# Kernel optimization log

Hardware: AMD Instinct MI355X
Metric: run time of the kernel (lower is better)

## Reference

```python
import jax, jax.numpy as jnp
import numpy as np

D_MODEL, D_INNER, D_STATE, D_CONV, DT_RANK = 2048, 4096, 16, 4, 128
B, T = 2, 1024


def setup_inputs() -> dict:
    key = jax.random.key(0)
    ks = jax.random.split(key, 8)
    dt_init_std = DT_RANK ** -0.5
    # dt bias init per the torch code: inv softplus of dt in [dt_min, dt_max]
    dt = jnp.exp(jax.random.uniform(ks[6], (D_INNER,)) * (np.log(0.1) - np.log(0.001)) + np.log(0.001))
    dt = jnp.clip(dt, 1e-4, None)
    dt_proj_b = dt + jnp.log(-jnp.expm1(-dt))
    A_log = jnp.log(jnp.tile(jnp.arange(1, D_STATE + 1, dtype=jnp.float32)[None, :], (D_INNER, 1)))
    return {
        "x": jax.random.normal(ks[0], (B, T, D_MODEL), jnp.float32),
        "h": jnp.zeros((B, D_INNER, D_STATE), jnp.float32),
        "conv_cache": jnp.zeros((B, D_INNER, D_CONV - 1), jnp.float32),
        "in_proj_w": jax.random.normal(ks[1], (2 * D_INNER, D_MODEL), jnp.float32) * 0.02,
        "conv_w": jax.random.normal(ks[2], (D_INNER, D_CONV), jnp.float32) * (1.0 / np.sqrt(D_CONV)),
        "conv_b": jnp.zeros((D_INNER,), jnp.float32),
        "x_proj_w": jax.random.normal(ks[3], (DT_RANK + 2 * D_STATE, D_INNER), jnp.float32) * 0.02,
        "dt_proj_w": jax.random.uniform(ks[4], (D_INNER, DT_RANK), jnp.float32, -dt_init_std, dt_init_std),
        "dt_proj_b": dt_proj_b,
        "A_log": A_log,
        "D_param": jnp.ones((D_INNER,), jnp.float32),
        "out_proj_w": jax.random.normal(ks[5], (D_MODEL, D_INNER), jnp.float32) * 0.02,
    }


def _forward(x, h, conv_cache, in_proj_w, conv_w, conv_b, x_proj_w,
             dt_proj_w, dt_proj_b, A_log, D_param, out_proj_w):
    Tlen = x.shape[1]
    xz = x @ in_proj_w.T                                  # (B,T,2*d_inner)
    xi, z = jnp.split(xz, 2, axis=-1)
    # causal depthwise conv with cache: concat history then valid conv
    xc = jnp.concatenate([jnp.swapaxes(conv_cache, 1, 2), xi], axis=1)  # (B,T+3,d_inner)
    new_conv_cache = jnp.swapaxes(xc[:, -(D_CONV - 1):, :], 1, 2)       # (B,d_inner,3)
    xconv = sum(xc[:, k:k + Tlen, :] * conv_w[:, k] for k in range(D_CONV)) + conv_b
    xs = jax.nn.silu(xconv)                               # (B,T,d_inner)
    # SSM params per step
    dbc = xs @ x_proj_w.T                                 # (B,T,dt_rank+2n)
    delta, Bm, Cm = jnp.split(dbc, [DT_RANK, DT_RANK + D_STATE], axis=-1)
    delta = jax.nn.softplus(delta @ dt_proj_w.T + dt_proj_b)  # (B,T,d_inner)
    A = -jnp.exp(A_log)                                   # (d_inner,n)
    dA = jnp.exp(jnp.einsum('btd,dn->btdn', delta, A))    # (B,T,d,n)
    dBx = jnp.einsum('btd,btn,btd->btdn', delta, Bm, xs)  # (B,T,d,n)

    def step(hc, inp):
        dA_t, dBx_t, C_t = inp
        hc = dA_t * hc + dBx_t                            # (B,d,n)
        return hc, jnp.einsum('bdn,bn->bd', hc, C_t)

    h_last, ys = jax.lax.scan(
        step, h,
        (jnp.moveaxis(dA, 1, 0), jnp.moveaxis(dBx, 1, 0), jnp.moveaxis(Cm, 1, 0)))
    y = jnp.moveaxis(ys, 0, 1) + D_param * xs             # (B,T,d_inner)
    out = (y * jax.nn.silu(z)) @ out_proj_w.T             # (B,T,d_model)
    return out, h_last, new_conv_cache


def reference(x, h, conv_cache, in_proj_w, conv_w, conv_b, x_proj_w,
              dt_proj_w, dt_proj_b, A_log, D_param, out_proj_w):
    return _forward(x, h, conv_cache, in_proj_w, conv_w, conv_b, x_proj_w,
                    dt_proj_w, dt_proj_b, A_log, D_param, out_proj_w)
```

## Files before the change

kernel.cpp:

```cpp
#include <hip/hip_runtime.h>
#include <hip/hip_bf16.h>
#include <math.h>

#define D_MODEL 2048
#define D_INNER 4096
#define D_STATE 16
#define D_CONV  4
#define DT_RANK 128
#define NB      2
#define TT      1024
#define M_TOT   (NB * TT)
#define NC      16
#define CL      64
#define TC      16

typedef __bf16 bf16x8_t __attribute__((ext_vector_type(8)));
typedef float  f32x4_t  __attribute__((ext_vector_type(4)));

__global__ __launch_bounds__(256) void fused_cast(
    const float* __restrict__ x,  const float* __restrict__ wi,
    const float* __restrict__ wo, const float* __restrict__ wx,
    const float* __restrict__ wdt,
    __bf16* __restrict__ x16,  __bf16* __restrict__ wi16,
    __bf16* __restrict__ wo16, __bf16* __restrict__ wx16,
    __bf16* __restrict__ wdt16, __bf16* __restrict__ dbc16,
    __bf16* __restrict__ out16)
{
    const size_t g = (size_t)blockIdx.x * 256 + threadIdx.x;
    const float* src; __bf16* dst; size_t off;
    if      (g < 524288)  { src = x;   dst = x16;   off = g; }
    else if (g < 2621440) { src = wi;  dst = wi16;  off = g - 524288; }
    else if (g < 3670016) { src = wo;  dst = wo16;  off = g - 2621440; }
    else if (g < 3801088) { off = g - 3670016; dst = wx16;
                            src = (g < 3751936) ? wx : nullptr; }
    else if (g < 3866624) { src = wdt; dst = wdt16; off = g - 3801088; }
    else if (g < 3948544) { src = nullptr; dst = dbc16; off = g - 3866624; }
    else                  { src = nullptr; dst = out16; off = g - 3948544; }

    bf16x8_t v;
    if (src) {
        const float4 f0 = ((const float4*)src)[2 * off];
        const float4 f1 = ((const float4*)src)[2 * off + 1];
        v[0] = (__bf16)f0.x; v[1] = (__bf16)f0.y; v[2] = (__bf16)f0.z; v[3] = (__bf16)f0.w;
        v[4] = (__bf16)f1.x; v[5] = (__bf16)f1.y; v[6] = (__bf16)f1.z; v[7] = (__bf16)f1.w;
    } else {
        v = (bf16x8_t)(__bf16)0.f;
    }
    ((bf16x8_t*)dst)[off] = v;
}

template <int EPI, int KSTEP, typename OutT>
__global__ __launch_bounds__(256) void gemm_bf16_nt(
    const __bf16* __restrict__ A, int lda,
    const __bf16* __restrict__ W, int ldw,
    OutT* __restrict__ C, int ldc,
    int Kloop, int Nmax, const float* __restrict__ bias)
{
    __shared__ __bf16 As[128 * KSTEP];
    __shared__ __bf16 Bs[128 * KSTEP];

    const int tid  = threadIdx.x;
    const int wave = tid >> 6;
    const int lane = tid & 63;
    const int m0 = blockIdx.y * 128;
    const int n0 = blockIdx.x * 128;
    const int mw = (wave >> 1) * 64;
    const int nw = (wave & 1) * 64;
    const int koff = blockIdx.z * Kloop;

    f32x4_t acc[4][4] = {};

    const int g0 = wave * 2;
    const int rA = g0 * 16 + (lane >> 2);
    const int kk = (lane & 3) * 8;

    const __bf16* gA0 = A + (size_t)(m0 + rA) * lda + kk + koff;
    const __bf16* gA1 = gA0 + (size_t)16 * lda;
    const __bf16* gB0 = W + (size_t)(n0 + rA) * ldw + kk + koff;
    const __bf16* gB1 = gB0 + (size_t)16 * ldw;

    __bf16* lA0 = &As[(size_t)g0 * 512];
    __bf16* lA1 = &As[(size_t)(g0 + 1) * 512];
    __bf16* lB0 = &Bs[(size_t)g0 * 512];
    __bf16* lB1 = &Bs[(size_t)(g0 + 1) * 512];

    const int fr = lane & 15;
    const int fk = (lane >> 4) * 8;

    for (int k0 = 0; k0 < Kloop; k0 += KSTEP) {
#pragma unroll
        for (int p = 0; p < KSTEP / 32; p++) {
            const int kp = k0 + p * 32;
            const int lp = p * 4096;
            __builtin_amdgcn_global_load_lds(
                (const __attribute__((address_space(1))) void*)(gA0 + kp),
                (__attribute__((address_space(3))) void*)(lA0 + lp), 16, 0, 0);
            __builtin_amdgcn_global_load_lds(
                (const __attribute__((address_space(1))) void*)(gA1 + kp),
                (__attribute__((address_space(3))) void*)(lA1 + lp), 16, 0, 0);
            __builtin_amdgcn_global_load_lds(
                (const __attribute__((address_space(1))) void*)(gB0 + kp),
                (__attribute__((address_space(3))) void*)(lB0 + lp), 16, 0, 0);
            __builtin_amdgcn_global_load_lds(
                (const __attribute__((address_space(1))) void*)(gB1 + kp),
                (__attribute__((address_space(3))) void*)(lB1 + lp), 16, 0, 0);
        }
        __syncthreads();

#pragma unroll
        for (int p = 0; p < KSTEP / 32; p++) {
            const int lp = p * 4096;
            bf16x8_t av[4], bv[4];
#pragma unroll
            for (int mt = 0; mt < 4; mt++)
                av[mt] = *(const bf16x8_t*)&As[lp + (mw + mt * 16 + fr) * 32 + fk];
#pragma unroll
            for (int nt = 0; nt < 4; nt++)
                bv[nt] = *(const bf16x8_t*)&Bs[lp + (nw + nt * 16 + fr) * 32 + fk];

#pragma unroll
            for (int mt = 0; mt < 4; mt++)
#pragma unroll
                for (int nt = 0; nt < 4; nt++)
                    acc[mt][nt] = __builtin_amdgcn_mfma_f32_16x16x32_bf16(
                        av[mt], bv[nt], acc[mt][nt], 0, 0, 0);
        }
        __syncthreads();
    }

    const int cn = n0 + nw + (lane & 15);
    const int rb = m0 + mw + (lane >> 4) * 4;
#pragma unroll
    for (int mt = 0; mt < 4; mt++)
#pragma unroll
        for (int nt = 0; nt < 4; nt++) {
            const int n = cn + nt * 16;
            if (n >= Nmax) continue;
#pragma unroll
            for (int r = 0; r < 4; r++) {
                float v = acc[mt][nt][r];
                OutT* p = &C[(size_t)(rb + mt * 16 + r) * ldc + n];
                if (EPI == 1) {
                    v += bias[n];
                    v = (v > 20.f) ? v : log1pf(__expf(v));
                    *p = (OutT)v;
                } else if (EPI == 2) {
                    atomicAdd((float*)p, v);
                } else {
                    *p = (OutT)v;
                }
            }
        }
}

__global__ __launch_bounds__(256) void gemm_dt(
    const float* __restrict__ A,
    const __bf16* __restrict__ W,
    __bf16* __restrict__ C,
    const float* __restrict__ bias)
{
    __shared__ __bf16 As[128 * 32];
    __shared__ __bf16 Bs[128 * 32];

    const int tid  = threadIdx.x;
    const int wave = tid >> 6;
    const int lane = tid & 63;
    const int m0 = blockIdx.y * 128;
    const int n0 = blockIdx.x * 128;
    const int mw = (wave >> 1) * 64;
    const int nw = (wave & 1) * 64;

    f32x4_t acc[4][4] = {};

    const int g0 = wave * 2;
    const int rA = g0 * 16 + (lane >> 2);
    const int kk = (lane & 3) * 8;

    const float*  gA0 = A + (size_t)(m0 + rA) * 160 + kk;
    const float*  gA1 = gA0 + (size_t)16 * 160;
    const __bf16* gB0 = W + (size_t)(n0 + rA) * 128 + kk;
    const __bf16* gB1 = gB0 + (size_t)16 * 128;

    __bf16* lA0 = &As[(size_t)g0 * 512];
    __bf16* lA1 = &As[(size_t)(g0 + 1) * 512];
    __bf16* lB0 = &Bs[(size_t)g0 * 512];
    __bf16* lB1 = &Bs[(size_t)(g0 + 1) * 512];

    const int fr = lane & 15;
    const int fk = (lane >> 4) * 8;

    for (int k0 = 0; k0 < 128; k0 += 32) {
        const float4 a0 = *(const float4*)(gA0 + k0);
        const float4 a1 = *(const float4*)(gA0 + k0 + 4);
        const float4 a2 = *(const float4*)(gA1 + k0);
        const float4 a3 = *(const float4*)(gA1 + k0 + 4);
        bf16x8_t va, vb;
        va[0] = (__bf16)a0.x; va[1] = (__bf16)a0.y; va[2] = (__bf16)a0.z; va[3] = (__bf16)a0.w;
        va[4] = (__bf16)a1.x; va[5] = (__bf16)a1.y; va[6] = (__bf16)a1.z; va[7] = (__bf16)a1.w;
        vb[0] = (__bf16)a2.x; vb[1] = (__bf16)a2.y; vb[2] = (__bf16)a2.z; vb[3] = (__bf16)a2.w;
        vb[4] = (__bf16)a3.x; vb[5] = (__bf16)a3.y; vb[6] = (__bf16)a3.z; vb[7] = (__bf16)a3.w;
        ((bf16x8_t*)lA0)[lane] = va;
        ((bf16x8_t*)lA1)[lane] = vb;
        __builtin_amdgcn_global_load_lds(
            (const __attribute__((address_space(1))) void*)(gB0 + k0),
            (__attribute__((address_space(3))) void*)lB0, 16, 0, 0);
        __builtin_amdgcn_global_load_lds(
            (const __attribute__((address_space(1))) void*)(gB1 + k0),
            (__attribute__((address_space(3))) void*)lB1, 16, 0, 0);
        __syncthreads();

        bf16x8_t av[4], bv[4];
#pragma unroll
        for (int mt = 0; mt < 4; mt++)
            av[mt] = *(const bf16x8_t*)&As[(mw + mt * 16 + fr) * 32 + fk];
#pragma unroll
        for (int nt = 0; nt < 4; nt++)
            bv[nt] = *(const bf16x8_t*)&Bs[(nw + nt * 16 + fr) * 32 + fk];

#pragma unroll
        for (int mt = 0; mt < 4; mt++)
#pragma unroll
            for (int nt = 0; nt < 4; nt++)
                acc[mt][nt] = __builtin_amdgcn_mfma_f32_16x16x32_bf16(
                    av[mt], bv[nt], acc[mt][nt], 0, 0, 0);
        __syncthreads();
    }

    const int cn = n0 + nw + (lane & 15);
    const int rb = m0 + mw + (lane >> 4) * 4;
#pragma unroll
    for (int mt = 0; mt < 4; mt++)
#pragma unroll
        for (int nt = 0; nt < 4; nt++) {
            const int n = cn + nt * 16;
            const float bs = bias[n];
#pragma unroll
            for (int r = 0; r < 4; r++) {
                float v = acc[mt][nt][r] + bs;
                v = (v > 20.f) ? v : log1pf(__expf(v));
                C[(size_t)(rb + mt * 16 + r) * 4096 + n] = (__bf16)v;
            }
        }
}

__global__ __launch_bounds__(256) void conv_silu(
    const __bf16* __restrict__ xz16,
    const float* __restrict__ conv_cache,
    const float* __restrict__ conv_w,
    const float* __restrict__ conv_b,
    __bf16* __restrict__ xs16,
    float* __restrict__ cc_out)
{
    const int b  = blockIdx.z;
    const int d  = blockIdx.y * 256 + threadIdx.x;
    const int t0 = blockIdx.x * TC;

    const float4 w  = *(const float4*)&conv_w[d * 4];
    const float bias = conv_b[d];

    float v[TC + 3];
    if (t0 == 0) {
        v[0] = conv_cache[(b * D_INNER + d) * 3 + 0];
        v[1] = conv_cache[(b * D_INNER + d) * 3 + 1];
        v[2] = conv_cache[(b * D_INNER + d) * 3 + 2];
    } else {
        v[0] = (float)xz16[(size_t)(b * TT + t0 - 3) * 8192 + d];
        v[1] = (float)xz16[(size_t)(b * TT + t0 - 2) * 8192 + d];
        v[2] = (float)xz16[(size_t)(b * TT + t0 - 1) * 8192 + d];
    }
#pragma unroll
    for (int k = 0; k < TC; k++)
        v[k + 3] = (float)xz16[(size_t)(b * TT + t0 + k) * 8192 + d];

#pragma unroll
    for (int k = 0; k < TC; k++) {
        float c = v[k] * w.x + v[k + 1] * w.y + v[k + 2] * w.z + v[k + 3] * w.w + bias;
        float s = c / (1.f + __expf(-c));
        xs16[(size_t)(b * TT + t0 + k) * 4096 + d] = (__bf16)s;
    }

    if (t0 + TC == TT) {
        cc_out[(b * D_INNER + d) * 3 + 0] = v[TC];
        cc_out[(b * D_INNER + d) * 3 + 1] = v[TC + 1];
        cc_out[(b * D_INNER + d) * 3 + 2] = v[TC + 2];
    }
}

__global__ __launch_bounds__(256) void scan_phase_a(
    const __bf16* __restrict__ delta16,
    const float* __restrict__ dbc,
    const __bf16* __restrict__ xs16,
    const float* __restrict__ A_log,
    float* __restrict__ P,
    float* __restrict__ S)
{
    const int idx = blockIdx.x * 256 + threadIdx.x;
    const int sub = idx & 3;
    const int d   = (idx >> 2) & 4095;
    const int c   = (idx >> 14) & (NC - 1);
    const int b   = idx >> 18;

    const float4 Af = *(const float4*)&A_log[d * 16 + sub * 4];
    const float Ad0 = -__expf(Af.x), Ad1 = -__expf(Af.y);
    const float Ad2 = -__expf(Af.z), Ad3 = -__expf(Af.w);

    const int t0 = c * CL;
    const __bf16* pdelta = delta16 + (size_t)(b * TT + t0) * 4096 + d;
    const __bf16* px     = xs16 + (size_t)(b * TT + t0) * 4096 + d;
    const float*  pB     = dbc + ((size_t)b * TT + t0) * 160 + 128 + sub * 4;

    float h0 = 0.f, h1 = 0.f, h2 = 0.f, h3 = 0.f, sd = 0.f;
#pragma unroll 4
    for (int t = 0; t < CL; t++) {
        const float delta = (float)pdelta[(size_t)t * 4096];
        const float xv    = (float)px[(size_t)t * 4096];
        const float4 Bv   = *(const float4*)&pB[(size_t)t * 160];
        const float dx = delta * xv;
        h0 = __expf(delta * Ad0) * h0 + dx * Bv.x;
        h1 = __expf(delta * Ad1) * h1 + dx * Bv.y;
        h2 = __expf(delta * Ad2) * h2 + dx * Bv.z;
        h3 = __expf(delta * Ad3) * h3 + dx * Bv.w;
        sd += delta;
    }
    const size_t o = ((size_t)(b * NC + c) * 4096 + d) * 16 + sub * 4;
    *(float4*)&P[o] = make_float4(__expf(Ad0 * sd), __expf(Ad1 * sd),
                                  __expf(Ad2 * sd), __expf(Ad3 * sd));
    *(float4*)&S[o] = make_float4(h0, h1, h2, h3);
}

__global__ __launch_bounds__(256) void scan_phase_c(
    const __bf16* __restrict__ delta16,
    const __bf16* __restrict__ xz16,
    const float* __restrict__ dbc,
    const __bf16* __restrict__ xs16,
    const float* __restrict__ P,
    const float* __restrict__ S,
    const float* __restrict__ h_in,
    const float* __restrict__ A_log,
    const float* __restrict__ D_param,
    __bf16* __restrict__ ys16,
    float* __restrict__ h_out)
{
    const int idx = blockIdx.x * 256 + threadIdx.x;
    const int sub = idx & 3;
    const int d   = (idx >> 2) & 4095;
    const int c   = (idx >> 14) & (NC - 1);
    const int b   = idx >> 18;

    const float4 Af = *(const float4*)&A_log[d * 16 + sub * 4];
    const float Ad0 = -__expf(Af.x), Ad1 = -__expf(Af.y);
    const float Ad2 = -__expf(Af.z), Ad3 = -__expf(Af.w);
    const float Dp = D_param[d];

    float4 hf = *(const float4*)&h_in[((size_t)b * 4096 + d) * 16 + sub * 4];
    float h0 = hf.x, h1 = hf.y, h2 = hf.z, h3 = hf.w;
    for (int cc = 0; cc < c; cc++) {
        const size_t o2 = ((size_t)(b * NC + cc) * 4096 + d) * 16 + sub * 4;
        const float4 p = *(const float4*)&P[o2];
        const float4 s = *(const float4*)&S[o2];
        h0 = p.x * h0 + s.x;
        h1 = p.y * h1 + s.y;
        h2 = p.z * h2 + s.z;
        h3 = p.w * h3 + s.w;
    }

    const int t0 = c * CL;
    const __bf16* pdelta = delta16 + (size_t)(b * TT + t0) * 4096 + d;
    const __bf16* pz     = xz16 + (size_t)(b * TT + t0) * 8192 + 4096 + d;
    const __bf16* px     = xs16 + (size_t)(b * TT + t0) * 4096 + d;
    const float*  pB     = dbc + ((size_t)b * TT + t0) * 160 + 128 + sub * 4;
    const float*  pC     = pB + 16;
    __bf16* py = ys16 + (size_t)(b * TT + t0) * 4096 + d;

#pragma unroll 4
    for (int t = 0; t < CL; t++) {
        const float delta = (float)pdelta[(size_t)t * 4096];
        const float xv    = (float)px[(size_t)t * 4096];
        const float4 Bv   = *(const float4*)&pB[(size_t)t * 160];
        const float4 Cv   = *(const float4*)&pC[(size_t)t * 160];
        const float dx = delta * xv;

        h0 = __expf(delta * Ad0) * h0 + dx * Bv.x;
        h1 = __expf(delta * Ad1) * h1 + dx * Bv.y;
        h2 = __expf(delta * Ad2) * h2 + dx * Bv.z;
        h3 = __expf(delta * Ad3) * h3 + dx * Bv.w;

        float y = h0 * Cv.x + h1 * Cv.y + h2 * Cv.z + h3 * Cv.w;
        y += __shfl_xor(y, 1);
        y += __shfl_xor(y, 2);

        if (sub == 0) {
            const float zv = (float)pz[(size_t)t * 8192];
            y += Dp * xv;
            const float g = zv / (1.f + __expf(-zv));
            py[(size_t)t * 4096] = (__bf16)(y * g);
        }
    }

    if (c == NC - 1) {
        *(float4*)&h_out[((size_t)b * 4096 + d) * 16 + sub * 4] =
            make_float4(h0, h1, h2, h3);
    }
}

extern "C" void kernel_launch(void* const* d_in, const int* in_sizes, int n_in,
                              void* d_out, int out_size, void* d_ws, size_t ws_size,
                              hipStream_t stream)
{
    const float* x          = (const float*)d_in[0];
    const float* h_in       = (const float*)d_in[1];
    const float* conv_cache = (const float*)d_in[2];
    const float* in_proj_w  = (const float*)d_in[3];
    const float* conv_w     = (const float*)d_in[4];
    const float* conv_b     = (const float*)d_in[5];
    const float* x_proj_w   = (const float*)d_in[6];
    const float* dt_proj_w  = (const float*)d_in[7];
    const float* dt_proj_b  = (const float*)d_in[8];
    const float* A_log      = (const float*)d_in[9];
    const float* D_param    = (const float*)d_in[10];
    const float* out_proj_w = (const float*)d_in[11];

    float* out    = (float*)d_out;
    float* h_out  = (float*)d_out + (size_t)NB * TT * D_MODEL;
    float* cc_out = h_out + (size_t)NB * D_INNER * D_STATE;

    char* ws = (char*)d_ws;
    __bf16* xz16    = (__bf16*)(ws);
    __bf16* x16     = (__bf16*)(ws + 33554432);
    float*  Pbuf    = (float*)(ws + 33554432);
    __bf16* wi16    = (__bf16*)(ws + 41943040);
    __bf16* delta16 = (__bf16*)(ws + 41943040);
    float*  Sbuf    = (float*)(ws + 58720256);
    __bf16* wo16    = (__bf16*)(ws + 75497472);
    __bf16* xs16    = (__bf16*)(ws + 92274688);
    float*  dbc     = (float*)(ws + 109051904);
    __bf16* ys16    = (__bf16*)(ws + 110362624);
    __bf16* wx16    = (__bf16*)(ws + 127139840);
    __bf16* wdt16   = (__bf16*)(ws + 129236992);

    dim3 blk(256);

    fused_cast<<<dim3(19520), blk, 0, stream>>>(
        x, in_proj_w, out_proj_w, x_proj_w, dt_proj_w,
        x16, wi16, wo16, wx16, wdt16, (__bf16*)dbc, (__bf16*)out);

    gemm_bf16_nt<0, 64, __bf16><<<dim3(64, 16, 1), blk, 0, stream>>>(
        x16, 2048, wi16, 2048, xz16, 8192, 2048, 8192, nullptr);

    conv_silu<<<dim3(TT / TC, D_INNER / 256, NB), blk, 0, stream>>>(
        xz16, conv_cache, conv_w, conv_b, xs16, cc_out);

    gemm_bf16_nt<2, 32, float><<<dim3(2, 16, 16), blk, 0, stream>>>(
        xs16, 4096, wx16, 4096, dbc, 160, 256, 160, nullptr);

    gemm_dt<<<dim3(32, 16), blk, 0, stream>>>(dbc, wdt16, delta16, dt_proj_b);

    scan_phase_a<<<dim3(NB * D_INNER * NC * 4 / 256), blk, 0, stream>>>(
        delta16, dbc, xs16, A_log, Pbuf, Sbuf);
    scan_phase_c<<<dim3(NB * D_INNER * NC * 4 / 256), blk, 0, stream>>>(
        delta16, xz16, dbc, xs16, Pbuf, Sbuf, h_in, A_log, D_param, ys16, h_out);

    gemm_bf16_nt<2, 64, float><<<dim3(16, 16, 2), blk, 0, stream>>>(
        ys16, 4096, wo16, 4096, out, 2048, 2048, 2048, nullptr);
}
```

Before: 489.3 us.

## Fuse all pipeline stages into one cooperative persistent kernel with grid syncs

Replaces the eight separate kernel launches with a single cooperative kernel of 1024 blocks that runs cast, in_proj GEMM, conv, x_proj GEMM, dt GEMM and both scan phases, separated by grid-wide syncs. The aim is to remove launch gaps and tail effects between stages. The final out_proj GEMM is remapped to 1024 blocks with split-K of 4 instead of 2. The conv tile length changes from 16 to 32 to match the block count. If the cooperative launch fails, the code falls back to the original multi-kernel sequence. The risks are grid.sync overhead, a launch bound of 4 blocks per CU that may limit registers, and shared memory sized for the largest stage in every stage.

```diff
diff --git a/kernel.cpp b/kernel.cpp
--- a/kernel.cpp
+++ b/kernel.cpp
@@ -1,32 +1,30 @@
 #include <hip/hip_runtime.h>
+#include <hip/hip_cooperative_groups.h>
 #include <hip/hip_bf16.h>
 #include <math.h>
 
 #define D_MODEL 2048
 #define D_INNER 4096
 #define D_STATE 16
-#define D_CONV  4
 #define DT_RANK 128
 #define NB      2
 #define TT      1024
 #define M_TOT   (NB * TT)
 #define NC      16
 #define CL      64
-#define TC      16
+#define CTC     32
 
 typedef __bf16 bf16x8_t __attribute__((ext_vector_type(8)));
 typedef float  f32x4_t  __attribute__((ext_vector_type(4)));
 
-__global__ __launch_bounds__(256) void fused_cast(
-    const float* __restrict__ x,  const float* __restrict__ wi,
-    const float* __restrict__ wo, const float* __restrict__ wx,
-    const float* __restrict__ wdt,
-    __bf16* __restrict__ x16,  __bf16* __restrict__ wi16,
-    __bf16* __restrict__ wo16, __bf16* __restrict__ wx16,
-    __bf16* __restrict__ wdt16, __bf16* __restrict__ dbc16,
-    __bf16* __restrict__ out16)
-{
-    const size_t g = (size_t)blockIdx.x * 256 + threadIdx.x;
+
+__device__ __forceinline__ void dev_cast(
+    size_t g,
+    const float* x,  const float* wi, const float* wo, const float* wx,
+    const float* wdt,
+    __bf16* x16, __bf16* wi16, __bf16* wo16, __bf16* wx16,
+    __bf16* wdt16, __bf16* dbc16, __bf16* out16)
+{
     const float* src; __bf16* dst; size_t off;
     if      (g < 524288)  { src = x;   dst = x16;   off = g; }
     else if (g < 2621440) { src = wi;  dst = wi16;  off = g - 524288; }
@@ -50,23 +48,20 @@
 }
 
 template <int EPI, int KSTEP, typename OutT>
-__global__ __launch_bounds__(256) void gemm_bf16_nt(
+__device__ __forceinline__ void dev_gemm(
     const __bf16* __restrict__ A, int lda,
     const __bf16* __restrict__ W, int ldw,
     OutT* __restrict__ C, int ldc,
-    int Kloop, int Nmax, const float* __restrict__ bias)
-{
-    __shared__ __bf16 As[128 * KSTEP];
-    __shared__ __bf16 Bs[128 * KSTEP];
-
-    const int tid  = threadIdx.x;
+    int Kloop, int Nmax, const float* __restrict__ bias,
+    int bx, int by, int bz, __bf16* As, __bf16* Bs, int tid)
+{
     const int wave = tid >> 6;
     const int lane = tid & 63;
-    const int m0 = blockIdx.y * 128;
-    const int n0 = blockIdx.x * 128;
+    const int m0 = by * 128;
+    const int n0 = bx * 128;
     const int mw = (wave >> 1) * 64;
     const int nw = (wave & 1) * 64;
-    const int koff = blockIdx.z * Kloop;
+    const int koff = bz * Kloop;
 
     f32x4_t acc[4][4] = {};
 
@@ -79,10 +74,10 @@
     const __bf16* gB0 = W + (size_t)(n0 + rA) * ldw + kk + koff;
     const __bf16* gB1 = gB0 + (size_t)16 * ldw;
 
-    __bf16* lA0 = &As[(size_t)g0 * 512];
-    __bf16* lA1 = &As[(size_t)(g0 + 1) * 512];
-    __bf16* lB0 = &Bs[(size_t)g0 * 512];
-    __bf16* lB1 = &Bs[(size_t)(g0 + 1) * 512];
+    __bf16* lA0 = As + (size_t)g0 * 512;
+    __bf16* lA1 = As + (size_t)(g0 + 1) * 512;
+    __bf16* lB0 = Bs + (size_t)g0 * 512;
+    __bf16* lB1 = Bs + (size_t)(g0 + 1) * 512;
 
     const int fr = lane & 15;
     const int fk = (lane >> 4) * 8;
@@ -153,20 +148,17 @@
         }
 }
 
-__global__ __launch_bounds__(256) void gemm_dt(
+__device__ __forceinline__ void dev_dt(
     const float* __restrict__ A,
     const __bf16* __restrict__ W,
     __bf16* __restrict__ C,
-    const float* __restrict__ bias)
-{
-    __shared__ __bf16 As[128 * 32];
-    __shared__ __bf16 Bs[128 * 32];
-
-    const int tid  = threadIdx.x;
+    const float* __restrict__ bias,
+    int bx, int by, __bf16* As, __bf16* Bs, int tid)
+{
     const int wave = tid >> 6;
     const int lane = tid & 63;
-    const int m0 = blockIdx.y * 128;
-    const int n0 = blockIdx.x * 128;
+    const int m0 = by * 128;
+    const int n0 = bx * 128;
     const int mw = (wave >> 1) * 64;
     const int nw = (wave & 1) * 64;
 
@@ -181,10 +173,10 @@
     const __bf16* gB0 = W + (size_t)(n0 + rA) * 128 + kk;
     const __bf16* gB1 = gB0 + (size_t)16 * 128;
 
-    __bf16* lA0 = &As[(size_t)g0 * 512];
-    __bf16* lA1 = &As[(size_t)(g0 + 1) * 512];
-    __bf16* lB0 = &Bs[(size_t)g0 * 512];
-    __bf16* lB1 = &Bs[(size_t)(g0 + 1) * 512];
+    __bf16* lA0 = As + (size_t)g0 * 512;
+    __bf16* lA1 = As + (size_t)(g0 + 1) * 512;
+    __bf16* lB0 = Bs + (size_t)g0 * 512;
+    __bf16* lB1 = Bs + (size_t)(g0 + 1) * 512;
 
     const int fr = lane & 15;
     const int fk = (lane >> 4) * 8;
@@ -243,22 +235,22 @@
         }
 }
 
-__global__ __launch_bounds__(256) void conv_silu(
+__device__ __forceinline__ void dev_conv(
     const __bf16* __restrict__ xz16,
     const float* __restrict__ conv_cache,
     const float* __restrict__ conv_w,
     const float* __restrict__ conv_b,
     __bf16* __restrict__ xs16,
-    float* __restrict__ cc_out)
-{
-    const int b  = blockIdx.z;
-    const int d  = blockIdx.y * 256 + threadIdx.x;
-    const int t0 = blockIdx.x * TC;
+    float* __restrict__ cc_out, int bid, int tid)
+{
+    const int t0 = (bid & 31) * CTC;
+    const int d  = (((bid >> 5) & 15) << 8) + tid;
+    const int b  = bid >> 9;
 
     const float4 w  = *(const float4*)&conv_w[d * 4];
     const float bias = conv_b[d];
 
-    float v[TC + 3];
+    float v[CTC + 3];
     if (t0 == 0) {
         v[0] = conv_cache[(b * D_INNER + d) * 3 + 0];
         v[1] = conv_cache[(b * D_INNER + d) * 3 + 1];
@@ -269,32 +261,31 @@
         v[2] = (float)xz16[(size_t)(b * TT + t0 - 1) * 8192 + d];
     }
 #pragma unroll
-    for (int k = 0; k < TC; k++)
+    for (int k = 0; k < CTC; k++)
         v[k + 3] = (float)xz16[(size_t)(b * TT + t0 + k) * 8192 + d];
 
 #pragma unroll
-    for (int k = 0; k < TC; k++) {
+    for (int k = 0; k < CTC; k++) {
         float c = v[k] * w.x + v[k + 1] * w.y + v[k + 2] * w.z + v[k + 3] * w.w + bias;
         float s = c / (1.f + __expf(-c));
         xs16[(size_t)(b * TT + t0 + k) * 4096 + d] = (__bf16)s;
     }
 
-    if (t0 + TC == TT) {
-        cc_out[(b * D_INNER + d) * 3 + 0] = v[TC];
-        cc_out[(b * D_INNER + d) * 3 + 1] = v[TC + 1];
-        cc_out[(b * D_INNER + d) * 3 + 2] = v[TC + 2];
-    }
-}
-
-__global__ __launch_bounds__(256) void scan_phase_a(
+    if (t0 + CTC == TT) {
+        cc_out[(b * D_INNER + d) * 3 + 0] = v[CTC];
+        cc_out[(b * D_INNER + d) * 3 + 1] = v[CTC + 1];
+        cc_out[(b * D_INNER + d) * 3 + 2] = v[CTC + 2];
+    }
+}
+
+__device__ __forceinline__ void dev_scanA(
+    int idx,
     const __bf16* __restrict__ delta16,
     const float* __restrict__ dbc,
     const __bf16* __restrict__ xs16,
     const float* __restrict__ A_log,
-    float* __restrict__ P,
-    float* __restrict__ S)
-{
-    const int idx = blockIdx.x * 256 + threadIdx.x;
+    float* __restrict__ P, float* __restrict__ S)
+{
     const int sub = idx & 3;
     const int d   = (idx >> 2) & 4095;
     const int c   = (idx >> 14) & (NC - 1);
@@ -328,20 +319,18 @@
     *(float4*)&S[o] = make_float4(h0, h1, h2, h3);
 }
 
-__global__ __launch_bounds__(256) void scan_phase_c(
+__device__ __forceinline__ void dev_scanC(
+    int idx,
     const __bf16* __restrict__ delta16,
     const __bf16* __restrict__ xz16,
     const float* __restrict__ dbc,
     const __bf16* __restrict__ xs16,
-    const float* __restrict__ P,
-    const float* __restrict__ S,
+    const float* __restrict__ P, const float* __restrict__ S,
     const float* __restrict__ h_in,
     const float* __restrict__ A_log,
     const float* __restrict__ D_param,
-    __bf16* __restrict__ ys16,
-    float* __restrict__ h_out)
-{
-    const int idx = blockIdx.x * 256 + threadIdx.x;
+    __bf16* __restrict__ ys16, float* __restrict__ h_out)
+{
     const int sub = idx & 3;
     const int d   = (idx >> 2) & 4095;
     const int c   = (idx >> 14) & (NC - 1);
@@ -401,6 +390,112 @@
         *(float4*)&h_out[((size_t)b * 4096 + d) * 16 + sub * 4] =
             make_float4(h0, h1, h2, h3);
     }
+}
+
+struct MegaArgs {
+    const float *x, *wi, *wo, *wx, *wdt;
+    const float *h_in, *conv_cache, *conv_w, *conv_b, *dt_proj_b, *A_log, *D_param;
+    float *out, *h_out, *cc_out;
+    __bf16 *xz16, *x16, *wi16, *wo16, *xs16, *ys16, *wx16, *wdt16, *delta16;
+    float *dbc, *P, *S;
+};
+
+__global__ __launch_bounds__(256, 4) void mega(MegaArgs a)
+{
+    cooperative_groups::grid_group grid = cooperative_groups::this_grid();
+    __shared__ __bf16 As[128 * 64];
+    __shared__ __bf16 Bs[128 * 64];
+    const int tid = threadIdx.x;
+    const int bid = blockIdx.x;
+
+    for (size_t g = (size_t)bid * 256 + tid; g < 4997120; g += 262144)
+        dev_cast(g, a.x, a.wi, a.wo, a.wx, a.wdt,
+                 a.x16, a.wi16, a.wo16, a.wx16, a.wdt16,
+                 (__bf16*)a.dbc, (__bf16*)a.out);
+    grid.sync();
+
+    dev_gemm<0, 64, __bf16>(a.x16, 2048, a.wi16, 2048, a.xz16, 8192,
+                            2048, 8192, nullptr, bid & 63, bid >> 6, 0, As, Bs, tid);
+    grid.sync();
+
+    dev_conv(a.xz16, a.conv_cache, a.conv_w, a.conv_b, a.xs16, a.cc_out, bid, tid);
+    grid.sync();
+
+    if (bid < 512)
+        dev_gemm<2, 32, float>(a.xs16, 4096, a.wx16, 4096, a.dbc, 160,
+                               256, 160, nullptr, bid & 1, (bid >> 1) & 15, bid >> 5,
+                               As, Bs, tid);
+    grid.sync();
+
+    if (bid < 512)
+        dev_dt(a.dbc, a.wdt16, a.delta16, a.dt_proj_b, bid & 31, bid >> 5, As, Bs, tid);
+    grid.sync();
+
+    dev_scanA(bid * 256 + tid,          a.delta16, a.dbc, a.xs16, a.A_log, a.P, a.S);
+    dev_scanA(bid * 256 + tid + 262144, a.delta16, a.dbc, a.xs16, a.A_log, a.P, a.S);
+    grid.sync();
+
+    dev_scanC(bid * 256 + tid,          a.delta16, a.xz16, a.dbc, a.xs16, a.P, a.S,
+              a.h_in, a.A_log, a.D_param, a.ys16, a.h_out);
+    dev_scanC(bid * 256 + tid + 262144, a.delta16, a.xz16, a.dbc, a.xs16, a.P, a.S,
+              a.h_in, a.A_log, a.D_param, a.ys16, a.h_out);
+    grid.sync();
+
+    dev_gemm<2, 64, float>(a.ys16, 4096, a.wo16, 4096, a.out, 2048,
+                           1024, 2048, nullptr, bid & 15, (bid >> 4) & 15, bid >> 8,
+                           As, Bs, tid);
+}
+
+__global__ __launch_bounds__(256) void k_cast(
+    const float* x, const float* wi, const float* wo, const float* wx,
+    const float* wdt, __bf16* x16, __bf16* wi16, __bf16* wo16, __bf16* wx16,
+    __bf16* wdt16, __bf16* dbc16, __bf16* out16)
+{
+    dev_cast((size_t)blockIdx.x * 256 + threadIdx.x,
+             x, wi, wo, wx, wdt, x16, wi16, wo16, wx16, wdt16, dbc16, out16);
+}
+
+template <int EPI, int KSTEP, typename OutT>
+__global__ __launch_bounds__(256) void k_gemm(
+    const __bf16* A, int lda, const __bf16* W, int ldw,
+    OutT* C, int ldc, int Kloop, int Nmax, const float* bias)
+{
+    __shared__ __bf16 As[128 * KSTEP];
+    __shared__ __bf16 Bs[128 * KSTEP];
+    dev_gemm<EPI, KSTEP, OutT>(A, lda, W, ldw, C, ldc, Kloop, Nmax, bias,
+                               blockIdx.x, blockIdx.y, blockIdx.z, As, Bs, threadIdx.x);
+}
+
+__global__ __launch_bounds__(256) void k_dt(
+    const float* A, const __bf16* W, __bf16* C, const float* bias)
+{
+    __shared__ __bf16 As[128 * 32];
+    __shared__ __bf16 Bs[128 * 32];
+    dev_dt(A, W, C, bias, blockIdx.x, blockIdx.y, As, Bs, threadIdx.x);
+}
+
+__global__ __launch_bounds__(256) void k_conv(
+    const __bf16* xz16, const float* conv_cache, const float* conv_w,
+    const float* conv_b, __bf16* xs16, float* cc_out)
+{
+    dev_conv(xz16, conv_cache, conv_w, conv_b, xs16, cc_out,
+             blockIdx.x, threadIdx.x);
+}
+
+__global__ __launch_bounds__(256) void k_scanA(
+    const __bf16* delta16, const float* dbc, const __bf16* xs16,
+    const float* A_log, float* P, float* S)
+{
+    dev_scanA(blockIdx.x * 256 + threadIdx.x, delta16, dbc, xs16, A_log, P, S);
+}
+
+__global__ __launch_bounds__(256) void k_scanC(
+    const __bf16* delta16, const __bf16* xz16, const float* dbc,
+    const __bf16* xs16, const float* P, const float* S, const float* h_in,
+    const float* A_log, const float* D_param, __bf16* ys16, float* h_out)
+{
+    dev_scanC(blockIdx.x * 256 + threadIdx.x, delta16, xz16, dbc, xs16, P, S,
+              h_in, A_log, D_param, ys16, h_out);
 }
 
 extern "C" void kernel_launch(void* const* d_in, const int* in_sizes, int n_in,
@@ -438,28 +533,36 @@
     __bf16* wx16    = (__bf16*)(ws + 127139840);
     __bf16* wdt16   = (__bf16*)(ws + 129236992);
 
-    dim3 blk(256);
-
-    fused_cast<<<dim3(19520), blk, 0, stream>>>(
-        x, in_proj_w, out_proj_w, x_proj_w, dt_proj_w,
-        x16, wi16, wo16, wx16, wdt16, (__bf16*)dbc, (__bf16*)out);
-
-    gemm_bf16_nt<0, 64, __bf16><<<dim3(64, 16, 1), blk, 0, stream>>>(
-        x16, 2048, wi16, 2048, xz16, 8192, 2048, 8192, nullptr);
-
-    conv_silu<<<dim3(TT / TC, D_INNER / 256, NB), blk, 0, stream>>>(
-        xz16, conv_cache, conv_w, conv_b, xs16, cc_out);
-
-    gemm_bf16_nt<2, 32, float><<<dim3(2, 16, 16), blk, 0, stream>>>(
-        xs16, 4096, wx16, 4096, dbc, 160, 256, 160, nullptr);
-
-    gemm_dt<<<dim3(32, 16), blk, 0, stream>>>(dbc, wdt16, delta16, dt_proj_b);
-
-    scan_phase_a<<<dim3(NB * D_INNER * NC * 4 / 256), blk, 0, stream>>>(
-        delta16, dbc, xs16, A_log, Pbuf, Sbuf);
-    scan_phase_c<<<dim3(NB * D_INNER * NC * 4 / 256), blk, 0, stream>>>(
-        delta16, xz16, dbc, xs16, Pbuf, Sbuf, h_in, A_log, D_param, ys16, h_out);
-
-    gemm_bf16_nt<2, 64, float><<<dim3(16, 16, 2), blk, 0, stream>>>(
-        ys16, 4096, wo16, 4096, out, 2048, 2048, 2048, nullptr);
-}
+    MegaArgs ma;
+    ma.x = x; ma.wi = in_proj_w; ma.wo = out_proj_w; ma.wx = x_proj_w; ma.wdt = dt_proj_w;
+    ma.h_in = h_in; ma.conv_cache = conv_cache; ma.conv_w = conv_w; ma.conv_b = conv_b;
+    ma.dt_proj_b = dt_proj_b; ma.A_log = A_log; ma.D_param = D_param;
+    ma.out = out; ma.h_out = h_out; ma.cc_out = cc_out;
+    ma.xz16 = xz16; ma.x16 = x16; ma.wi16 = wi16; ma.wo16 = wo16; ma.xs16 = xs16;
+    ma.ys16 = ys16; ma.wx16 = wx16; ma.wdt16 = wdt16; ma.delta16 = delta16;
+    ma.dbc = dbc; ma.P = Pbuf; ma.S = Sbuf;
+
+    void* kp[] = { (void*)&ma };
+    hipError_t ce = hipLaunchCooperativeKernel(
+        (const void*)mega, dim3(1024), dim3(256), kp, 0, stream);
+
+    if (ce != hipSuccess) {
+        (void)hipGetLastError();
+        dim3 blk(256);
+        k_cast<<<dim3(19520), blk, 0, stream>>>(
+            x, in_proj_w, out_proj_w, x_proj_w, dt_proj_w,
+            x16, wi16, wo16, wx16, wdt16, (__bf16*)dbc, (__bf16*)out);
+        k_gemm<0, 64, __bf16><<<dim3(64, 16, 1), blk, 0, stream>>>(
+            x16, 2048, wi16, 2048, xz16, 8192, 2048, 8192, nullptr);
+        k_conv<<<dim3(1024), blk, 0, stream>>>(
+            xz16, conv_cache, conv_w, conv_b, xs16, cc_out);
+        k_gemm<2, 32, float><<<dim3(2, 16, 16), blk, 0, stream>>>(
+            xs16, 4096, wx16, 4096, dbc, 160, 256, 160, nullptr);
+        k_dt<<<dim3(32, 16), blk, 0, stream>>>(dbc, wdt16, delta16, dt_proj_b);
+        k_scanA<<<dim3(2048), blk, 0, stream>>>(delta16, dbc, xs16, A_log, Pbuf, Sbuf);
+        k_scanC<<<dim3(2048), blk, 0, stream>>>(
+            delta16, xz16, dbc, xs16, Pbuf, Sbuf, h_in, A_log, D_param, ys16, h_out);
+        k_gemm<2, 64, float><<<dim3(16, 16, 2), blk, 0, stream>>>(
+            ys16, 4096, wo16, 4096, out, 2048, 2048, 2048, nullptr);
+    }
+}
```

Result: slower. 1.365 ms (+179.0%).
